# Kernel tuning notes

Measured on AMD Instinct MI355X. Metric: run time of the kernel, lower is better.

## Reference

```python
import jax, jax.numpy as jnp
import numpy as np

N_NODES = 100000
N_EDGES = 1600000
IN_CH = 128
HID = 64
HEADS = 2
OUT_CH = 2
EDGE_DIM = 3
NEG_SLOPE = 0.2
EPS = 1e-16  # PyG softmax denominator epsilon


def gat_conv(x, edge_index, edge_attr, W, We, att_src, att_dst, att_edge, bias, heads, out_ch, concat):
    """Faithful PyG GATConv (edge_dim enabled, eval mode, add_self_loops handled by caller=False here
    since the repo passes raw edge_index; PyG default add_self_loops=True is intentionally mirrored below)."""
    N = x.shape[0]
    src, dst = edge_index[0], edge_index[1]
    H, C = heads, out_ch
    h = (x @ W).reshape(N, H, C)                    # [N,H,C] node projections
    e = (edge_attr @ We).reshape(-1, H, C)          # [E,H,C] edge projections
    a_src = jnp.sum(h * att_src, axis=-1)           # [N,H]
    a_dst = jnp.sum(h * att_dst, axis=-1)           # [N,H]
    alpha = a_src[src] + a_dst[dst] + jnp.sum(e * att_edge, axis=-1)  # [E,H]
    alpha = jax.nn.leaky_relu(alpha, NEG_SLOPE)
    # segment softmax over incoming edges of each dst node
    amax = jax.ops.segment_max(alpha, dst, num_segments=N)            # [N,H]
    amax = jnp.where(jnp.isfinite(amax), amax, 0.0)
    alpha = jnp.exp(alpha - amax[dst])
    denom = jax.ops.segment_sum(alpha, dst, num_segments=N)           # [N,H]
    alpha = alpha / (denom[dst] + EPS)
    msg = h[src] * alpha[:, :, None]                                  # [E,H,C]
    out = jax.ops.segment_sum(msg, dst, num_segments=N)               # [N,H,C]
    if concat:
        out = out.reshape(N, H * C)
    else:
        out = out.mean(axis=1)
    return out + bias


def add_self_loops(edge_index, edge_attr, n):
    loops = jnp.arange(n, dtype=edge_index.dtype)
    ei = jnp.concatenate([edge_index, jnp.stack([loops, loops])], axis=1)
    ea = jnp.concatenate([edge_attr, jnp.zeros((n, edge_attr.shape[1]), edge_attr.dtype)], axis=0)
    return ei, ea


def setup_inputs() -> dict:
    key = jax.random.key(0)
    ks = jax.random.split(key, 16)
    s = 0.1
    x = jax.random.normal(ks[0], (N_NODES, IN_CH), jnp.float32)
    edge_index = jax.random.randint(ks[1], (2, N_EDGES), 0, N_NODES, jnp.int64 if jax.config.jax_enable_x64 else jnp.int32)
    edge_feat = jax.random.normal(ks[2], (N_EDGES, EDGE_DIM), jnp.float32)
    HC = HEADS * HID
    return {
        "x": x, "edge_index": edge_index, "edge_feat": edge_feat,
        "W1": jax.random.normal(ks[3], (IN_CH, HC), jnp.float32) * s,
        "We1": jax.random.normal(ks[4], (EDGE_DIM, HC), jnp.float32) * s,
        "as1": jax.random.normal(ks[5], (1, HEADS, HID), jnp.float32) * s,
        "ad1": jax.random.normal(ks[6], (1, HEADS, HID), jnp.float32) * s,
        "ae1": jax.random.normal(ks[7], (1, HEADS, HID), jnp.float32) * s,
        "b1": jnp.zeros((HC,), jnp.float32),
        "W2": jax.random.normal(ks[8], (HC, OUT_CH), jnp.float32) * s,
        "We2": jax.random.normal(ks[9], (EDGE_DIM, OUT_CH), jnp.float32) * s,
        "as2": jax.random.normal(ks[10], (1, 1, OUT_CH), jnp.float32) * s,
        "ad2": jax.random.normal(ks[11], (1, 1, OUT_CH), jnp.float32) * s,
        "ae2": jax.random.normal(ks[12], (1, 1, OUT_CH), jnp.float32) * s,
        "b2": jnp.zeros((OUT_CH,), jnp.float32),
    }


def reference(x, edge_index, edge_feat, W1, We1, as1, ad1, ae1, b1, W2, We2, as2, ad2, ae2, b2):
    # eval mode: F.dropout is identity
    ei, ea = add_self_loops(edge_index, edge_feat, x.shape[0])  # PyG GATConv default add_self_loops=True
    h = gat_conv(x, ei, ea, W1, We1, as1, ad1, ae1, b1, HEADS, HID, concat=True)
    h = jax.nn.elu(h)
    out = gat_conv(h, ei, ea, W2, We2, as2, ad2, ae2, b2, 1, OUT_CH, concat=False)
    return out
```

## Files before the change

kernel.cpp:

```cpp
#include <hip/hip_runtime.h>
#include <hip/hip_bf16.h>

#define NN 100000
#define NE 1600000
#define NEG_SLOPE 0.2f
#define GEPS 1e-16f
#define WSHIFT 4.0f

#define HB 64
#define EB (NE / HB)
#define HPASS 4
#define HBIN 25000
#define HBW (HBIN / 2)
#define CAPS ((size_t)(NE + 8 * NN))

#define SRCMASK 0x1FFFFu

#define EDGE_BLKS ((NE / 4 + 255) / 256)
#define FILL_BLKS ((NN + 255) / 256)

typedef __attribute__((ext_vector_type(8))) short short8;
typedef __attribute__((ext_vector_type(4))) float f32x4;
typedef __attribute__((ext_vector_type(2))) _Float16 h2v;

__device__ __forceinline__ unsigned short f2b(float f) {
  unsigned u = __float_as_uint(f);
  u += 0x7fffu + ((u >> 16) & 1u);
  return (unsigned short)(u >> 16);
}
__device__ __forceinline__ unsigned short f2h(float f) {
  _Float16 h = (_Float16)f;
  return __builtin_bit_cast(unsigned short, h);
}
__device__ __forceinline__ float h2f(unsigned short u) {
  return (float)__builtin_bit_cast(_Float16, u);
}
__device__ __forceinline__ unsigned pkh2(float lo, float hi) {
  return (unsigned)f2h(lo) | ((unsigned)f2h(hi) << 16);
}
__device__ __forceinline__ float dot2h(unsigned a, unsigned b, float c) {
  return __builtin_amdgcn_fdot2(__builtin_bit_cast(h2v, a), __builtin_bit_cast(h2v, b), c, false);
}
__device__ __forceinline__ unsigned permb(unsigned s0, unsigned s1, int sel) {
  return __builtin_amdgcn_perm(s0, s1, sel);
}
__device__ __forceinline__ unsigned pkSE(int src, float ez) {
  return (unsigned)src | ((unsigned)(f2h(ez) >> 1) << 17);
}
__device__ __forceinline__ float unpkEZ(unsigned y) {
  return h2f((unsigned short)((y >> 17) << 1));
}
#define HSEL_LO 0x05040100
#define HSEL_HI 0x07060302
#define ONE2    0x3C003C00u
#define EZPAD   (-60000.0f)

__global__ void k_prep(const float* __restrict__ We1, const float* __restrict__ ae1,
                       const float* __restrict__ We2, const float* __restrict__ ae2,
                       const float* __restrict__ W1, const float* __restrict__ as1,
                       const float* __restrict__ ad1,
                       float* __restrict__ q, float4* __restrict__ pq) {
  int t = threadIdx.x;
  if (t < 6) {
    int d = t >> 1, hh = t & 1;
    float s = 0.f;
    for (int c = 0; c < 64; ++c) s += We1[d * 128 + hh * 64 + c] * ae1[hh * 64 + c];
    q[t] = s;
  } else if (t < 9) {
    int d = t - 6;
    q[8 + d] = We2[d * 2 + 0] * ae2[0] + We2[d * 2 + 1] * ae2[1];
  }
  if (t < 128) {
    float s0 = 0.f, s1 = 0.f, d0 = 0.f, d1 = 0.f;
    for (int c = 0; c < 64; ++c) {
      float w0 = W1[t * 128 + c], w1 = W1[t * 128 + 64 + c];
      s0 += w0 * as1[c];      s1 += w1 * as1[64 + c];
      d0 += w0 * ad1[c];      d1 += w1 * ad1[64 + c];
    }
    pq[t] = make_float4(s0, s1, d0, d1);
  }
}

__global__ __launch_bounds__(512, 4) void k_gemm(const float* __restrict__ x,
                                                 const float* __restrict__ W,
                                                 const float4* __restrict__ pq,
                                                 unsigned short* __restrict__ h1b,
                                                 float* __restrict__ a1s,
                                                 float* __restrict__ a1d) {
  __shared__ unsigned short xa[128 * 128];
  __shared__ unsigned short wt[128 * 128];
  int t = threadIdx.x;
  int row0 = blockIdx.x * 128;

  {
    int kr = t >> 2, n0 = (t & 3) * 32;
    const float* wp = &W[kr * 128 + n0];
    int cb = kr >> 3, klo = kr & 7;
#pragma unroll
    for (int j = 0; j < 8; ++j) {
      float4 v = *(const float4*)&wp[j * 4];
      int n = n0 + j * 4;
      wt[(n + 0) * 128 + ((cb ^ ((n + 0) & 15)) * 8) + klo] = f2b(v.x);
      wt[(n + 1) * 128 + ((cb ^ ((n + 1) & 15)) * 8) + klo] = f2b(v.y);
      wt[(n + 2) * 128 + ((cb ^ ((n + 2) & 15)) * 8) + klo] = f2b(v.z);
      wt[(n + 3) * 128 + ((cb ^ ((n + 3) & 15)) * 8) + klo] = f2b(v.w);
    }
  }
  {
    int lrow = t >> 2, qq = t & 3;
    int grow = row0 + lrow; if (grow >= NN) grow = NN - 1;
    const float* xp = &x[(size_t)grow * 128 + qq * 32];
    const float4* pqp = &pq[qq * 32];
    float ps0 = 0.f, ps1 = 0.f, pd0 = 0.f, pd1 = 0.f;
    int sw = lrow & 15;
#pragma unroll
    for (int j = 0; j < 4; ++j) {
      float4 u = *(const float4*)&xp[j * 8];
      float4 v = *(const float4*)&xp[j * 8 + 4];
      float xs[8] = {u.x, u.y, u.z, u.w, v.x, v.y, v.z, v.w};
      short8 sv;
#pragma unroll
      for (int e = 0; e < 8; ++e) {
        float4 pv = pqp[j * 8 + e];
        ps0 += xs[e] * pv.x; ps1 += xs[e] * pv.y;
        pd0 += xs[e] * pv.z; pd1 += xs[e] * pv.w;
        sv[e] = (short)f2b(xs[e]);
      }
      int c = qq * 4 + j;
      *(short8*)&xa[lrow * 128 + ((c ^ sw) * 8)] = sv;
    }
    ps0 += __shfl_xor(ps0, 1); ps0 += __shfl_xor(ps0, 2);
    ps1 += __shfl_xor(ps1, 1); ps1 += __shfl_xor(ps1, 2);
    pd0 += __shfl_xor(pd0, 1); pd0 += __shfl_xor(pd0, 2);
    pd1 += __shfl_xor(pd1, 1); pd1 += __shfl_xor(pd1, 2);
    if (qq == 0) {
      *(float2*)&a1s[grow * 2] = make_float2(ps0, ps1);
      *(float2*)&a1d[grow * 2] = make_float2(pd0, pd1);
    }
  }
  __syncthreads();

  int lane = t & 63, w = t >> 6;
  int m = lane & 15, quad = lane >> 4;
  int wm = (w & 1) * 64, wn = (w >> 1) * 32;
  f32x4 acc[4][2];
#pragma unroll
  for (int mi = 0; mi < 4; ++mi)
#pragma unroll
    for (int ni = 0; ni < 2; ++ni) acc[mi][ni] = (f32x4)(0.f);

#pragma unroll
  for (int kk = 0; kk < 4; ++kk) {
    int c = kk * 4 + quad;
    int co = (c ^ m) * 8;
    short8 a[4], b[2];
#pragma unroll
    for (int mi = 0; mi < 4; ++mi)
      a[mi] = *(const short8*)&xa[(wm + mi * 16 + m) * 128 + co];
#pragma unroll
    for (int ni = 0; ni < 2; ++ni)
      b[ni] = *(const short8*)&wt[(wn + ni * 16 + m) * 128 + co];
#pragma unroll
    for (int mi = 0; mi < 4; ++mi)
#pragma unroll
      for (int ni = 0; ni < 2; ++ni)
        acc[mi][ni] = __builtin_amdgcn_mfma_f32_16x16x32_bf16(a[mi], b[ni], acc[mi][ni], 0, 0, 0);
  }
#pragma unroll
  for (int mi = 0; mi < 4; ++mi)
#pragma unroll
    for (int r = 0; r < 4; ++r) {
      int grow = row0 + wm + mi * 16 + quad * 4 + r;
      if (grow >= NN) grow = NN - 1;
#pragma unroll
      for (int ni = 0; ni < 2; ++ni)
        h1b[(size_t)grow * 128 + wn + ni * 16 + m] = f2h(acc[mi][ni][r]);
    }
}

__global__ __launch_bounds__(1024) void k_hist(const int* __restrict__ ei,
                                               unsigned short* __restrict__ off16,
                                               unsigned short* __restrict__ rank) {
  __shared__ unsigned cnt[HBW];
  int b = blockIdx.x >> 2;
  int pass = blockIdx.x & 3;
  int base = pass * HBIN;
  int t = threadIdx.x;
  for (int i = t; i < HBW; i += 1024) cnt[i] = 0;
  __syncthreads();
  const int* dsts = &ei[NE + b * EB];
  for (int i = t * 4; i < EB; i += 4096) {
    int4 d = *(const int4*)&dsts[i];
    int dv[4] = {d.x, d.y, d.z, d.w};
#pragma unroll
    for (int j = 0; j < 4; ++j) {
      int rel = dv[j] - base;
      if ((unsigned)rel < (unsigned)HBIN) {
        unsigned sh = (unsigned)(rel & 1) << 4;
        unsigned old = atomicAdd(&cnt[rel >> 1], 1u << sh);
        rank[b * EB + i + j] = (unsigned short)((old >> sh) & 0xffffu);
      }
    }
  }
  __syncthreads();
  unsigned short* dp = &off16[(size_t)b * NN + base];
  for (int i = t; i < HBW; i += 1024) *(unsigned*)&dp[i * 2] = cnt[i];
}

__global__ void k_sumdeg(unsigned short* __restrict__ off16, int* __restrict__ deg) {
  int n = blockIdx.x * 256 + threadIdx.x;
  if (n >= NN) return;
  int run = 0;
#pragma unroll
  for (int b = 0; b < HB; ++b) {
    size_t idx = (size_t)b * NN + n;
    int c = off16[idx];
    off16[idx] = (unsigned short)run;
    run += c;
  }
  deg[n] = run;
}

__device__ __forceinline__ int padlen(int d) { return (d + 8) & ~7; }

__global__ void k_scan1(const int* __restrict__ deg, int* __restrict__ bsum) {
  __shared__ int lds[256];
  int t = threadIdx.x;
  int base = blockIdx.x * 1024 + t * 4;
  int s = 0;
  for (int j = 0; j < 4; ++j) { int i = base + j; s += (i < NN) ? padlen(deg[i]) : 0; }
  lds[t] = s; __syncthreads();
  for (int o = 128; o > 0; o >>= 1) { if (t < o) lds[t] += lds[t + o]; __syncthreads(); }
  if (t == 0) bsum[blockIdx.x] = lds[0];
}

__global__ void k_scan2(int* __restrict__ bsum, int nb) {
  __shared__ int lds[128];
  int t = threadIdx.x;
  int v = (t < nb) ? bsum[t] : 0;
  lds[t] = v; __syncthreads();
  for (int o = 1; o < 128; o <<= 1) {
    int u = (t >= o) ? lds[t - o] : 0;
    __syncthreads();
    lds[t] += u;
    __syncthreads();
  }
  if (t < nb) bsum[t] = lds[t] - v;
}

__global__ void k_scan3(const int* __restrict__ deg, const int* __restrict__ bbase,
                        int* __restrict__ rowptr) {
  __shared__ int lds[256];
  int t = threadIdx.x;
  int base = blockIdx.x * 1024 + t * 4;
  int v[4]; int s = 0;
  for (int j = 0; j < 4; ++j) { int i = base + j; v[j] = (i < NN) ? padlen(deg[i]) : 0; s += v[j]; }
  lds[t] = s; __syncthreads();
  for (int o = 1; o < 256; o <<= 1) {
    int u = (t >= o) ? lds[t - o] : 0;
    __syncthreads();
    lds[t] += u;
    __syncthreads();
  }
  int excl = lds[t] - s + bbase[blockIdx.x];
  for (int j = 0; j < 4; ++j) {
    int i = base + j;
    if (i <= NN) rowptr[i] = excl;
    excl += v[j];
  }
}

__global__ void k_scatter(const int* __restrict__ ei, const float* __restrict__ ef,
                          const float* __restrict__ a1s, const float* __restrict__ a1d,
                          const float* __restrict__ q, const int* __restrict__ rowptr,
                          const int* __restrict__ deg,
                          const unsigned short* __restrict__ rank,
                          const unsigned short* __restrict__ off16,
                          float2* __restrict__ cpk1) {
  int bid = blockIdx.x;
  if (bid < EDGE_BLKS) {
    int t4 = bid * 256 + threadIdx.x;
    if (t4 >= NE / 4) return;
    int e0 = t4 * 4;
    int hb = e0 / EB;
    const unsigned short* offp = &off16[(size_t)hb * NN];
    int4 ss = *(const int4*)&ei[e0];
    int4 dd = *(const int4*)&ei[NE + e0];
    ushort4 rk = *(const ushort4*)&rank[e0];
    float4 fA = *(const float4*)&ef[e0 * 3];
    float4 fB = *(const float4*)&ef[e0 * 3 + 4];
    float4 fC = *(const float4*)&ef[e0 * 3 + 8];
    float f[4][3] = {{fA.x, fA.y, fA.z}, {fA.w, fB.x, fB.y},
                     {fB.z, fB.w, fC.x}, {fC.y, fC.z, fC.w}};
    int src[4] = {ss.x, ss.y, ss.z, ss.w};
    int dst[4] = {dd.x, dd.y, dd.z, dd.w};
    int rnk[4] = {rk.x, rk.y, rk.z, rk.w};
#pragma unroll
    for (int j = 0; j < 4; ++j) {
      float e0h = f[j][0] * q[0] + f[j][1] * q[2] + f[j][2] * q[4];
      float e1h = f[j][0] * q[1] + f[j][1] * q[3] + f[j][2] * q[5];
      float ez  = f[j][0] * q[8] + f[j][1] * q[9] + f[j][2] * q[10];
      float al0 = a1s[src[j] * 2] + a1d[dst[j] * 2] + e0h;
      float al1 = a1s[src[j] * 2 + 1] + a1d[dst[j] * 2 + 1] + e1h;
      al0 = al0 > 0.f ? al0 : NEG_SLOPE * al0;
      al1 = al1 > 0.f ? al1 : NEG_SLOPE * al1;
      int pos = rowptr[dst[j]] + 1 + (int)offp[dst[j]] + rnk[j];
      cpk1[pos] = make_float2(
          __uint_as_float(pkh2(__expf(al0 - WSHIFT), __expf(al1 - WSHIFT))),
          __uint_as_float(pkSE(src[j], ez)));
    }
  } else {
    int n = (bid - EDGE_BLKS) * 256 + threadIdx.x;
    if (n >= NN) return;
    int s0 = rowptr[n];
    int d = deg[n];
    int pl = padlen(d);
    float2 sv = *(const float2*)&a1s[n * 2];
    float2 dv = *(const float2*)&a1d[n * 2];
    float al0 = sv.x + dv.x;
    float al1 = sv.y + dv.y;
    al0 = al0 > 0.f ? al0 : NEG_SLOPE * al0;
    al1 = al1 > 0.f ? al1 : NEG_SLOPE * al1;
    cpk1[s0] = make_float2(
        __uint_as_float(pkh2(__expf(al0 - WSHIFT), __expf(al1 - WSHIFT))),
        __uint_as_float(pkSE(n, 0.f)));
    float2 pad = make_float2(0.f, __uint_as_float(pkSE(n, EZPAD)));
    for (int k = 1 + d; k < pl; ++k) cpk1[s0 + k] = pad;
  }
}

__global__ __launch_bounds__(256) void k_agg1(const unsigned short* __restrict__ h1b,
                                              const int* __restrict__ rowptr,
                                              const float2* __restrict__ cpk1,
                                              const float* __restrict__ b1,
                                              const float* __restrict__ W2,
                                              const float* __restrict__ as2,
                                              const float* __restrict__ ad2,
                                              float4* __restrict__ nd) {
  int n = (int)((blockIdx.x * 256 + threadIdx.x) >> 6);
  int lane = threadIdx.x & 63;
  if (n >= NN) return;
  int s0 = rowptr[n], s1 = rowptr[n + 1];
  int g = lane >> 4;
  int lp = lane & 15;
  int wsel = (lp >= 8) ? HSEL_HI : HSEL_LO;

  float acc[8];
#pragma unroll
  for (int j = 0; j < 8; ++j) acc[j] = 0.f;
  float den = 0.f;

  int i = s0;
  for (; i + 16 <= s1; i += 16) {
    const float4* pp = (const float4*)(cpk1 + i + 4 * g);
    float4 p01 = pp[0];
    float4 p23 = pp[1];
    uint4 vA = *((const uint4*)(h1b + ((size_t)(__float_as_uint(p01.y) & SRCMASK) << 7)) + lp);
    uint4 vB = *((const uint4*)(h1b + ((size_t)(__float_as_uint(p01.w) & SRCMASK) << 7)) + lp);
    uint4 vC = *((const uint4*)(h1b + ((size_t)(__float_as_uint(p23.y) & SRCMASK) << 7)) + lp);
    uint4 vD = *((const uint4*)(h1b + ((size_t)(__float_as_uint(p23.w) & SRCMASK) << 7)) + lp);
    unsigned wAB = permb(__float_as_uint(p01.z), __float_as_uint(p01.x), wsel);
    unsigned wCD = permb(__float_as_uint(p23.z), __float_as_uint(p23.x), wsel);
    den = dot2h(wAB, ONE2, den);
    den = dot2h(wCD, ONE2, den);
    acc[0] = dot2h(permb(vB.x, vA.x, HSEL_LO), wAB, acc[0]);
    acc[1] = dot2h(permb(vB.x, vA.x, HSEL_HI), wAB, acc[1]);
    acc[2] = dot2h(permb(vB.y, vA.y, HSEL_LO), wAB, acc[2]);
    acc[3] = dot2h(permb(vB.y, vA.y, HSEL_HI), wAB, acc[3]);
    acc[4] = dot2h(permb(vB.z, vA.z, HSEL_LO), wAB, acc[4]);
    acc[5] = dot2h(permb(vB.z, vA.z, HSEL_HI), wAB, acc[5]);
    acc[6] = dot2h(permb(vB.w, vA.w, HSEL_LO), wAB, acc[6]);
    acc[7] = dot2h(permb(vB.w, vA.w, HSEL_HI), wAB, acc[7]);
    acc[0] = dot2h(permb(vD.x, vC.x, HSEL_LO), wCD, acc[0]);
    acc[1] = dot2h(permb(vD.x, vC.x, HSEL_HI), wCD, acc[1]);
    acc[2] = dot2h(permb(vD.y, vC.y, HSEL_LO), wCD, acc[2]);
    acc[3] = dot2h(permb(vD.y, vC.y, HSEL_HI), wCD, acc[3]);
    acc[4] = dot2h(permb(vD.z, vC.z, HSEL_LO), wCD, acc[4]);
    acc[5] = dot2h(permb(vD.z, vC.z, HSEL_HI), wCD, acc[5]);
    acc[6] = dot2h(permb(vD.w, vC.w, HSEL_LO), wCD, acc[6]);
    acc[7] = dot2h(permb(vD.w, vC.w, HSEL_HI), wCD, acc[7]);
  }
  if (i < s1) {
    float4 p = *(const float4*)(cpk1 + i + 2 * g);
    uint4 vA = *((const uint4*)(h1b + ((size_t)(__float_as_uint(p.y) & SRCMASK) << 7)) + lp);
    uint4 vB = *((const uint4*)(h1b + ((size_t)(__float_as_uint(p.w) & SRCMASK) << 7)) + lp);
    unsigned wAB = permb(__float_as_uint(p.z), __float_as_uint(p.x), wsel);
    den = dot2h(wAB, ONE2, den);
    acc[0] = dot2h(permb(vB.x, vA.x, HSEL_LO), wAB, acc[0]);
    acc[1] = dot2h(permb(vB.x, vA.x, HSEL_HI), wAB, acc[1]);
    acc[2] = dot2h(permb(vB.y, vA.y, HSEL_LO), wAB, acc[2]);
    acc[3] = dot2h(permb(vB.y, vA.y, HSEL_HI), wAB, acc[3]);
    acc[4] = dot2h(permb(vB.z, vA.z, HSEL_LO), wAB, acc[4]);
    acc[5] = dot2h(permb(vB.z, vA.z, HSEL_HI), wAB, acc[5]);
    acc[6] = dot2h(permb(vB.w, vA.w, HSEL_LO), wAB, acc[6]);
    acc[7] = dot2h(permb(vB.w, vA.w, HSEL_HI), wAB, acc[7]);
  }
#pragma unroll
  for (int o = 16; o <= 32; o <<= 1) {
    den += __shfl_xor(den, o);
#pragma unroll
    for (int j = 0; j < 8; ++j) acc[j] += __shfl_xor(acc[j], o);
  }
  float4 bA = *(const float4*)&b1[lp * 8];
  float4 bB = *(const float4*)&b1[lp * 8 + 4];
  float bb[8] = {bA.x, bA.y, bA.z, bA.w, bB.x, bB.y, bB.z, bB.w};
  float inv = 1.f / (den + GEPS);
  float r[8];
#pragma unroll
  for (int j = 0; j < 8; ++j) {
    float v = acc[j] * inv + bb[j];
    r[j] = v > 0.f ? v : __expf(v) - 1.f;
  }
  float4 wA = *(const float4*)&W2[lp * 16];
  float4 wB = *(const float4*)&W2[lp * 16 + 4];
  float4 wC = *(const float4*)&W2[lp * 16 + 8];
  float4 wD = *(const float4*)&W2[lp * 16 + 12];
  float p20 = r[0] * wA.x + r[1] * wA.z + r[2] * wB.x + r[3] * wB.z
            + r[4] * wC.x + r[5] * wC.z + r[6] * wD.x + r[7] * wD.z;
  float p21 = r[0] * wA.y + r[1] * wA.w + r[2] * wB.y + r[3] * wB.w
            + r[4] * wC.y + r[5] * wC.w + r[6] * wD.y + r[7] * wD.w;
#pragma unroll
  for (int o = 1; o <= 8; o <<= 1) { p20 += __shfl_xor(p20, o); p21 += __shfl_xor(p21, o); }
  if (lane == 0) {
    float4 v;
    v.x = p20; v.y = p21;
    v.z = p20 * as2[0] + p21 * as2[1];
    v.w = p20 * ad2[0] + p21 * ad2[1];
    nd[n] = v;
  }
}

__global__ __launch_bounds__(256) void k_agg2(const int* __restrict__ rowptr,
                                              const float2* __restrict__ cpk1,
                                              const float4* __restrict__ nd,
                                              const float* __restrict__ b2,
                                              float* __restrict__ out) {
  int wid = (int)((blockIdx.x * 256 + threadIdx.x) >> 6);
  int lane = threadIdx.x & 63;
  int g = lane >> 4, lp = lane & 15;
  int n = wid * 4 + g;
  if (n >= NN) return;
  int s0 = rowptr[n], s1 = rowptr[n + 1];
  float adn = nd[n].w;
  float den = 0.f, acc0 = 0.f, acc1 = 0.f;
  for (int i = s0 + lp; i < s1; i += 16) {
    float2 pk = cpk1[i];
    unsigned y = __float_as_uint(pk.y);
    int s = (int)(y & SRCMASK);
    float ezv = unpkEZ(y);
    float4 ns = nd[s];
    float v = ns.z + adn + ezv;
    v = v > 0.f ? v : NEG_SLOPE * v;
    float p = __expf(v);
    den += p;
    acc0 += p * ns.x;
    acc1 += p * ns.y;
  }
#pragma unroll
  for (int o = 1; o <= 8; o <<= 1) {
    den += __shfl_xor(den, o);
    acc0 += __shfl_xor(acc0, o);
    acc1 += __shfl_xor(acc1, o);
  }
  if (lp == 0) {
    float2 r;
    r.x = acc0 / (den + GEPS) + b2[0];
    r.y = acc1 / (den + GEPS) + b2[1];
    *(float2*)&out[n * 2] = r;
  }
}

extern "C" void kernel_launch(void* const* d_in, const int* in_sizes, int n_in,
                              void* d_out, int out_size, void* d_ws, size_t ws_size,
                              hipStream_t stream) {
  (void)in_sizes; (void)n_in; (void)out_size; (void)ws_size;
  const float* x   = (const float*)d_in[0];
  const int*   ei  = (const int*)d_in[1];
  const float* ef  = (const float*)d_in[2];
  const float* W1  = (const float*)d_in[3];
  const float* We1 = (const float*)d_in[4];
  const float* as1 = (const float*)d_in[5];
  const float* ad1 = (const float*)d_in[6];
  const float* ae1 = (const float*)d_in[7];
  const float* b1  = (const float*)d_in[8];
  const float* W2  = (const float*)d_in[9];
  const float* We2 = (const float*)d_in[10];
  const float* as2 = (const float*)d_in[11];
  const float* ad2 = (const float*)d_in[12];
  const float* ae2 = (const float*)d_in[13];
  const float* b2  = (const float*)d_in[14];
  float* out = (float*)d_out;

  char* w = (char*)d_ws;
  auto alloc = [&](size_t bytes) -> char* {
    char* p = w; w += (bytes + 255) & ~(size_t)255; return p;
  };
  unsigned short* h1b = (unsigned short*)alloc((size_t)NN * 128 * 2);
  float*  a1s    = (float*)alloc((size_t)NN * 2 * 4);
  float*  a1d    = (float*)alloc((size_t)NN * 2 * 4);
  float4* nd     = (float4*)alloc((size_t)NN * 16);
  float*  q      = (float*)alloc(64);
  float4* pq     = (float4*)alloc(128 * 16);
  int*    deg    = (int*)alloc((size_t)NN * 4);
  int*    rowptr = (int*)alloc((size_t)(NN + 1) * 4);
  unsigned short* rank  = (unsigned short*)alloc((size_t)NE * 2);
  unsigned short* off16 = (unsigned short*)alloc((size_t)HB * NN * 2);
  int*    bsum   = (int*)alloc(128 * 4);
  float2* cpk1   = (float2*)alloc(CAPS * 8);

  const int NB_SCAN = (NN + 1023) / 1024;

  hipLaunchKernelGGL(k_prep, dim3(1), dim3(128), 0, stream,
                     We1, ae1, We2, ae2, W1, as1, ad1, q, pq);
  hipLaunchKernelGGL(k_gemm, dim3((NN + 127) / 128), dim3(512), 0, stream,
                     x, W1, pq, h1b, a1s, a1d);
  hipLaunchKernelGGL(k_hist, dim3(HB * HPASS), dim3(1024), 0, stream, ei, off16, rank);
  hipLaunchKernelGGL(k_sumdeg, dim3((NN + 255) / 256), dim3(256), 0, stream, off16, deg);
  hipLaunchKernelGGL(k_scan1, dim3(NB_SCAN), dim3(256), 0, stream, deg, bsum);
  hipLaunchKernelGGL(k_scan2, dim3(1), dim3(128), 0, stream, bsum, NB_SCAN);
  hipLaunchKernelGGL(k_scan3, dim3(NB_SCAN), dim3(256), 0, stream, deg, bsum, rowptr);
  hipLaunchKernelGGL(k_scatter, dim3(EDGE_BLKS + FILL_BLKS), dim3(256), 0, stream,
                     ei, ef, a1s, a1d, q, rowptr, deg, rank, off16, cpk1);
  hipLaunchKernelGGL(k_agg1, dim3((NN * 64 + 255) / 256), dim3(256), 0, stream,
                     h1b, rowptr, cpk1, b1, W2, as2, ad2, nd);
  hipLaunchKernelGGL(k_agg2, dim3(((NN + 3) / 4 * 64 + 255) / 256), dim3(256), 0, stream,
                     rowptr, cpk1, nd, b2, out);
}
```

Baseline: 343.8 us.

## Fuse histogram into GEMM launch, merge degree sum with scan, nontemporal edge loads

The edge-destination histogram blocks now share one launch with the node-projection GEMM blocks, using a union of shared memory, so the two independent workloads run concurrently instead of back-to-back. The per-node degree accumulation is fused into the first scan pass with vectorised ushort4 reads, which removes a launch and the separate read of deg. The streamed edge-record loads in both aggregation kernels become nontemporal so they are less likely to evict the gathered node features from cache. In exchange, the histogram blocks now run with 512 threads instead of 1024, and the combined kernel carries the GEMM's launch bounds and shared-memory footprint.

After: 336.4 us. 1.02x faster.

```diff
diff --git a/kernel.cpp b/kernel.cpp
--- a/kernel.cpp
+++ b/kernel.cpp
@@ -16,11 +16,15 @@
 
 #define SRCMASK 0x1FFFFu
 
+#define HIST_BLKS (HB * HPASS)
+#define GEMM_BLKS ((NN + 127) / 128)
+
 #define EDGE_BLKS ((NE / 4 + 255) / 256)
 #define FILL_BLKS ((NN + 255) / 256)
 
 typedef __attribute__((ext_vector_type(8))) short short8;
 typedef __attribute__((ext_vector_type(4))) float f32x4;
+typedef __attribute__((ext_vector_type(2))) float f32x2;
 typedef __attribute__((ext_vector_type(2))) _Float16 h2v;
 
 __device__ __forceinline__ unsigned short f2b(float f) {
@@ -49,6 +53,14 @@
 }
 __device__ __forceinline__ float unpkEZ(unsigned y) {
   return h2f((unsigned short)((y >> 17) << 1));
+}
+__device__ __forceinline__ float4 ntld4(const float4* p) {
+  f32x4 v = __builtin_nontemporal_load((const f32x4*)p);
+  float4 r; r.x = v.x; r.y = v.y; r.z = v.z; r.w = v.w; return r;
+}
+__device__ __forceinline__ float2 ntld2(const float2* p) {
+  f32x2 v = __builtin_nontemporal_load((const f32x2*)p);
+  float2 r; r.x = v.x; r.y = v.y; return r;
 }
 #define HSEL_LO 0x05040100
 #define HSEL_HI 0x07060302
@@ -81,16 +93,47 @@
   }
 }
 
-__global__ __launch_bounds__(512, 4) void k_gemm(const float* __restrict__ x,
-                                                 const float* __restrict__ W,
-                                                 const float4* __restrict__ pq,
-                                                 unsigned short* __restrict__ h1b,
-                                                 float* __restrict__ a1s,
-                                                 float* __restrict__ a1d) {
-  __shared__ unsigned short xa[128 * 128];
-  __shared__ unsigned short wt[128 * 128];
+__global__ __launch_bounds__(512, 4) void k_gh(
+    const int* __restrict__ ei, unsigned short* __restrict__ off16,
+    unsigned short* __restrict__ rank,
+    const float* __restrict__ x, const float* __restrict__ W,
+    const float4* __restrict__ pq, unsigned short* __restrict__ h1b,
+    float* __restrict__ a1s, float* __restrict__ a1d) {
+  __shared__ union SM {
+    struct { unsigned short xa[128 * 128]; unsigned short wt[128 * 128]; } g;
+    unsigned cnt[HBW];
+  } sm;
   int t = threadIdx.x;
-  int row0 = blockIdx.x * 128;
+
+  if (blockIdx.x < HIST_BLKS) {
+    int b = blockIdx.x >> 2;
+    int pass = blockIdx.x & 3;
+    int base = pass * HBIN;
+    for (int i = t; i < HBW; i += 512) sm.cnt[i] = 0;
+    __syncthreads();
+    const int* dsts = &ei[NE + b * EB];
+    for (int i = t * 4; i < EB; i += 2048) {
+      int4 d = *(const int4*)&dsts[i];
+      int dv[4] = {d.x, d.y, d.z, d.w};
+#pragma unroll
+      for (int j = 0; j < 4; ++j) {
+        int rel = dv[j] - base;
+        if ((unsigned)rel < (unsigned)HBIN) {
+          unsigned sh = (unsigned)(rel & 1) << 4;
+          unsigned old = atomicAdd(&sm.cnt[rel >> 1], 1u << sh);
+          rank[b * EB + i + j] = (unsigned short)((old >> sh) & 0xffffu);
+        }
+      }
+    }
+    __syncthreads();
+    unsigned short* dp = &off16[(size_t)b * NN + base];
+    for (int i = t; i < HBW; i += 512) *(unsigned*)&dp[i * 2] = sm.cnt[i];
+    return;
+  }
+
+  unsigned short* xa = sm.g.xa;
+  unsigned short* wt = sm.g.wt;
+  int row0 = (int)(blockIdx.x - HIST_BLKS) * 128;
 
   {
     int kr = t >> 2, n0 = (t & 3) * 32;
@@ -178,57 +221,42 @@
     }
 }
 
-__global__ __launch_bounds__(1024) void k_hist(const int* __restrict__ ei,
-                                               unsigned short* __restrict__ off16,
-                                               unsigned short* __restrict__ rank) {
-  __shared__ unsigned cnt[HBW];
-  int b = blockIdx.x >> 2;
-  int pass = blockIdx.x & 3;
-  int base = pass * HBIN;
-  int t = threadIdx.x;
-  for (int i = t; i < HBW; i += 1024) cnt[i] = 0;
-  __syncthreads();
-  const int* dsts = &ei[NE + b * EB];
-  for (int i = t * 4; i < EB; i += 4096) {
-    int4 d = *(const int4*)&dsts[i];
-    int dv[4] = {d.x, d.y, d.z, d.w};
-#pragma unroll
-    for (int j = 0; j < 4; ++j) {
-      int rel = dv[j] - base;
-      if ((unsigned)rel < (unsigned)HBIN) {
-        unsigned sh = (unsigned)(rel & 1) << 4;
-        unsigned old = atomicAdd(&cnt[rel >> 1], 1u << sh);
-        rank[b * EB + i + j] = (unsigned short)((old >> sh) & 0xffffu);
-      }
-    }
-  }
-  __syncthreads();
-  unsigned short* dp = &off16[(size_t)b * NN + base];
-  for (int i = t; i < HBW; i += 1024) *(unsigned*)&dp[i * 2] = cnt[i];
-}
-
-__global__ void k_sumdeg(unsigned short* __restrict__ off16, int* __restrict__ deg) {
-  int n = blockIdx.x * 256 + threadIdx.x;
-  if (n >= NN) return;
-  int run = 0;
-#pragma unroll
-  for (int b = 0; b < HB; ++b) {
-    size_t idx = (size_t)b * NN + n;
-    int c = off16[idx];
-    off16[idx] = (unsigned short)run;
-    run += c;
-  }
-  deg[n] = run;
-}
-
 __device__ __forceinline__ int padlen(int d) { return (d + 8) & ~7; }
 
-__global__ void k_scan1(const int* __restrict__ deg, int* __restrict__ bsum) {
+__global__ void k_degscan(unsigned short* __restrict__ off16, int* __restrict__ deg,
+                          int* __restrict__ bsum) {
   __shared__ int lds[256];
   int t = threadIdx.x;
-  int base = blockIdx.x * 1024 + t * 4;
+  int n0 = blockIdx.x * 1024 + t * 4;
   int s = 0;
-  for (int j = 0; j < 4; ++j) { int i = base + j; s += (i < NN) ? padlen(deg[i]) : 0; }
+  if (n0 + 3 < NN) {
+    int run0 = 0, run1 = 0, run2 = 0, run3 = 0;
+    for (int b = 0; b < HB; ++b) {
+      size_t idx = (size_t)b * NN + n0;
+      ushort4 c = *(const ushort4*)&off16[idx];
+      ushort4 w;
+      w.x = (unsigned short)run0; w.y = (unsigned short)run1;
+      w.z = (unsigned short)run2; w.w = (unsigned short)run3;
+      *(ushort4*)&off16[idx] = w;
+      run0 += c.x; run1 += c.y; run2 += c.z; run3 += c.w;
+    }
+    *(int4*)&deg[n0] = make_int4(run0, run1, run2, run3);
+    s = padlen(run0) + padlen(run1) + padlen(run2) + padlen(run3);
+  } else {
+    for (int j = 0; j < 4; ++j) {
+      int n = n0 + j;
+      if (n >= NN) break;
+      int run = 0;
+      for (int b = 0; b < HB; ++b) {
+        size_t idx = (size_t)b * NN + n;
+        int c = off16[idx];
+        off16[idx] = (unsigned short)run;
+        run += c;
+      }
+      deg[n] = run;
+      s += padlen(run);
+    }
+  }
   lds[t] = s; __syncthreads();
   for (int o = 128; o > 0; o >>= 1) { if (t < o) lds[t] += lds[t + o]; __syncthreads(); }
   if (t == 0) bsum[blockIdx.x] = lds[0];
@@ -353,8 +381,8 @@
   int i = s0;
   for (; i + 16 <= s1; i += 16) {
     const float4* pp = (const float4*)(cpk1 + i + 4 * g);
-    float4 p01 = pp[0];
-    float4 p23 = pp[1];
+    float4 p01 = ntld4(pp);
+    float4 p23 = ntld4(pp + 1);
     uint4 vA = *((const uint4*)(h1b + ((size_t)(__float_as_uint(p01.y) & SRCMASK) << 7)) + lp);
     uint4 vB = *((const uint4*)(h1b + ((size_t)(__float_as_uint(p01.w) & SRCMASK) << 7)) + lp);
     uint4 vC = *((const uint4*)(h1b + ((size_t)(__float_as_uint(p23.y) & SRCMASK) << 7)) + lp);
@@ -381,7 +409,7 @@
     acc[7] = dot2h(permb(vD.w, vC.w, HSEL_HI), wCD, acc[7]);
   }
   if (i < s1) {
-    float4 p = *(const float4*)(cpk1 + i + 2 * g);
+    float4 p = ntld4((const float4*)(cpk1 + i + 2 * g));
     uint4 vA = *((const uint4*)(h1b + ((size_t)(__float_as_uint(p.y) & SRCMASK) << 7)) + lp);
     uint4 vB = *((const uint4*)(h1b + ((size_t)(__float_as_uint(p.w) & SRCMASK) << 7)) + lp);
     unsigned wAB = permb(__float_as_uint(p.z), __float_as_uint(p.x), wsel);
@@ -444,7 +472,7 @@
   float adn = nd[n].w;
   float den = 0.f, acc0 = 0.f, acc1 = 0.f;
   for (int i = s0 + lp; i < s1; i += 16) {
-    float2 pk = cpk1[i];
+    float2 pk = ntld2(&cpk1[i]);
     unsigned y = __float_as_uint(pk.y);
     int s = (int)(y & SRCMASK);
     float ezv = unpkEZ(y);
@@ -512,11 +540,9 @@
 
   hipLaunchKernelGGL(k_prep, dim3(1), dim3(128), 0, stream,
                      We1, ae1, We2, ae2, W1, as1, ad1, q, pq);
-  hipLaunchKernelGGL(k_gemm, dim3((NN + 127) / 128), dim3(512), 0, stream,
-                     x, W1, pq, h1b, a1s, a1d);
-  hipLaunchKernelGGL(k_hist, dim3(HB * HPASS), dim3(1024), 0, stream, ei, off16, rank);
-  hipLaunchKernelGGL(k_sumdeg, dim3((NN + 255) / 256), dim3(256), 0, stream, off16, deg);
-  hipLaunchKernelGGL(k_scan1, dim3(NB_SCAN), dim3(256), 0, stream, deg, bsum);
+  hipLaunchKernelGGL(k_gh, dim3(HIST_BLKS + GEMM_BLKS), dim3(512), 0, stream,
+                     ei, off16, rank, x, W1, pq, h1b, a1s, a1d);
+  hipLaunchKernelGGL(k_degscan, dim3(NB_SCAN), dim3(256), 0, stream, off16, deg, bsum);
   hipLaunchKernelGGL(k_scan2, dim3(1), dim3(128), 0, stream, bsum, NB_SCAN);
   hipLaunchKernelGGL(k_scan3, dim3(NB_SCAN), dim3(256), 0, stream, deg, bsum, rowptr);
   hipLaunchKernelGGL(k_scatter, dim3(EDGE_BLKS + FILL_BLKS), dim3(256), 0, stream,
```
